# Performance work log

Hardware: AMD Instinct MI355X
Metric: run time of the kernel (lower is better)

The kernel has to match this reference:

```python
import jax, jax.numpy as jnp
import numpy as np

F = 32          # conf['num_features']
G = 96          # voxel grid extent
N_VOX = 80000   # occupied input voxels
BN_EPS = 1e-5


def _encode(c):
    c = c.astype(np.int64) + 8
    return (c[:, 0] * 512 + c[:, 1]) * 512 + c[:, 2]


def _offsets(ks, dil):
    r = np.arange(-(ks // 2), ks // 2 + 1) * dil
    return np.stack(np.meshgrid(r, r, r, indexing='ij'), -1).reshape(-1, 3)


def _build_map(in_coords, out_coords, offsets):
    # For each kernel offset k and output voxel j, find input voxel index at
    # out_coords[j] + offsets[k]; sentinel = n_in / n_out when absent.
    n_in, n_out = len(in_coords), len(out_coords)
    keys = _encode(in_coords)
    order = np.argsort(keys).astype(np.int32)
    skeys = keys[order]
    K = len(offsets)
    in_map = np.full((K, n_out), n_in, np.int32)
    out_map = np.full((K, n_out), n_out, np.int32)
    base = np.arange(n_out, dtype=np.int32)
    for k, off in enumerate(offsets):
        q = _encode(out_coords + off)
        pos = np.clip(np.searchsorted(skeys, q), 0, n_in - 1)
        valid = skeys[pos] == q
        in_map[k] = np.where(valid, order[pos], n_in)
        out_map[k] = np.where(valid, base, n_out)
    return jnp.asarray(in_map), jnp.asarray(out_map)


def setup_inputs() -> dict:
    rng = np.random.default_rng(0)
    idx = rng.choice(G ** 3, size=N_VOX, replace=False)
    coords = np.stack(np.unravel_index(idx, (G, G, G)), 1).astype(np.int64)
    c2 = np.unique(coords // 2 * 2, axis=0)   # stride-2 coords (enc1 output)
    c4 = np.unique(coords // 4 * 4, axis=0)   # stride-4 coords (c_out.C)

    m1_in, m1_out = _build_map(coords, c2, _offsets(5, 1))  # k5 s2 conv
    m2_in, m2_out = _build_map(c2, c2, _offsets(3, 2))      # enc1 blocks
    m3_in, m3_out = _build_map(c2, c4, _offsets(3, 2))      # conv2 -> c_out.C
    m4_in, m4_out = _build_map(c4, c4, _offsets(3, 4))      # enc2 blocks

    key = jax.random.key(0)
    ks = jax.random.split(key, 8)
    s = 0.05
    return {
        'x_geo': jax.random.normal(ks[0], (N_VOX, 1), jnp.float32),
        'x_col': jax.random.uniform(ks[1], (N_VOX, 3), jnp.float32),
        'w0': jax.random.normal(ks[2], (125, 4, F), jnp.float32) * s,
        'w_e1': jax.random.normal(ks[3], (2, 2, 27, F, F), jnp.float32) * s,
        'g_e1': jnp.ones((2, 2, F), jnp.float32),
        'b_e1': jnp.zeros((2, 2, F), jnp.float32),
        'w2': jax.random.normal(ks[4], (27, F, 2 * F), jnp.float32) * s,
        'w_e2': jax.random.normal(ks[5], (2, 2, 27, 2 * F, 2 * F), jnp.float32) * s,
        'g_e2': jnp.ones((2, 2, 2 * F), jnp.float32),
        'b_e2': jnp.zeros((2, 2, 2 * F), jnp.float32),
        'm1_in': m1_in, 'm1_out': m1_out,
        'm2_in': m2_in, 'm2_out': m2_out,
        'm3_in': m3_in, 'm3_out': m3_out,
        'm4_in': m4_in, 'm4_out': m4_out,
    }


def sparse_conv(feats, W, in_map, out_map):
    # gather -> GEMM -> scatter per kernel offset (lax.scan over K offsets)
    n_out = out_map.shape[1]
    fpad = jnp.concatenate([feats, jnp.zeros((1, feats.shape[1]), feats.dtype)], 0)
    out0 = jnp.zeros((n_out + 1, W.shape[2]), feats.dtype)
    def step(acc, kmw):
        im, om, w = kmw
        return acc.at[om].add(fpad[im] @ w), None
    out, _ = jax.lax.scan(step, out0, (in_map, out_map, W))
    return out[:n_out]


def batch_norm(x, g, b):
    mu = x.mean(0)
    var = ((x - mu) ** 2).mean(0)
    return (x - mu) * jax.lax.rsqrt(var + BN_EPS) * g + b


def basic_block(x, w, g, b, in_map, out_map):
    # ME BasicBlock: conv-BN-ReLU-conv-BN + residual, ReLU
    y = jax.nn.relu(batch_norm(sparse_conv(x, w[0], in_map, out_map), g[0], b[0]))
    y = batch_norm(sparse_conv(y, w[1], in_map, out_map), g[1], b[1])
    return jax.nn.relu(y + x)


def reference(x_geo, x_col, w0, w_e1, g_e1, b_e1, w2, w_e2, g_e2, b_e2,
              m1_in, m1_out, m2_in, m2_out, m3_in, m3_out, m4_in, m4_out):
    x = jnp.concatenate([x_geo, x_col], axis=1)          # ME.cat -> 4 channels
    x = jax.nn.relu(sparse_conv(x, w0, m1_in, m1_out))   # k5 s2 conv + ReLU
    for i in range(2):                                   # enc1 residual blocks
        x = basic_block(x, w_e1[i], g_e1[i], b_e1[i], m2_in, m2_out)
    x = sparse_conv(x, w2, m3_in, m3_out)                # conv2 onto c_out.C
    for i in range(2):                                   # enc2 residual blocks
        x = basic_block(x, w_e2[i], g_e2[i], b_e2[i], m4_in, m4_out)
    return x
```

## Files before the change

kernel.cpp:

```cpp
#include <hip/hip_runtime.h>
#include <hip/hip_bf16.h>


typedef float f4 __attribute__((ext_vector_type(4)));
typedef short short8 __attribute__((ext_vector_type(8)));
typedef short short4v __attribute__((ext_vector_type(4)));

#define BN_EPS 1e-5f

static inline int ceil_div(int a, int b) { return (a + b - 1) / b; }

static __device__ inline float btof(short s) {
    unsigned u = ((unsigned)(unsigned short)s) << 16;
    float f;
    __builtin_memcpy(&f, &u, 4);
    return f;
}
static __device__ inline short ftob(float f) {
    __hip_bfloat16 h = __float2bfloat16(f);
    short s;
    __builtin_memcpy(&s, &h, 2);
    return s;
}

struct Seg {
    const float* W;
    long long begin, end;
    int K, CIN, COUT;
};
struct ProArgs {
    Seg s[10];
    const float* geo;
    const float* col;
    __hip_bfloat16* x0;
    int n_vox;
    float* stats;
    __hip_bfloat16* pads[5];
    int padn[5];
    long long wf_total;
    __hip_bfloat16* Wf;
};

__global__ __launch_bounds__(256) void prologue(ProArgs pa, long long total) {
    long long e = (long long)blockIdx.x * 256 + threadIdx.x;
    if (e >= total) return;
    if (e < pa.wf_total) {
        int si = 0;
#pragma unroll
        for (int i = 0; i < 10; ++i)
            if (e >= pa.s[i].end) si = i + 1;
        const Seg sg = pa.s[si];
        long long r = e - sg.begin;
        int j = (int)(r & 7);
        int lane = (int)((r >> 3) & 63);
        long long rest = r >> 9;
        int NT = sg.COUT >> 4;
        int ntile = (int)(rest % NT);
        int chunk = (int)(rest / NT);
        int kd = chunk * 32 + ((lane >> 4) << 3) + j;
        int koff = kd / sg.CIN;
        int ci = kd % sg.CIN;
        int n = ntile * 16 + (lane & 15);
        float v = (koff < sg.K) ? sg.W[((size_t)koff * sg.CIN + ci) * sg.COUT + n] : 0.f;
        pa.Wf[e] = __float2bfloat16(v);
        return;
    }
    long long r = e - pa.wf_total;
    if (r < pa.n_vox) {
        int row = (int)r;
        pa.x0[row * 4 + 0] = __float2bfloat16(pa.geo[row]);
        pa.x0[row * 4 + 1] = __float2bfloat16(pa.col[row * 3 + 0]);
        pa.x0[row * 4 + 2] = __float2bfloat16(pa.col[row * 3 + 1]);
        pa.x0[row * 4 + 3] = __float2bfloat16(pa.col[row * 3 + 2]);
        return;
    }
    r -= pa.n_vox;
    if (r < 4096) {
        pa.stats[r] = 0.f;
        return;
    }
    r -= 4096;
#pragma unroll
    for (int i = 0; i < 5; ++i) {
        if (r < pa.padn[i]) {
            pa.pads[i][r] = __float2bfloat16(0.f);
            return;
        }
        r -= pa.padn[i];
    }
}

template <int C>
__device__ inline void bn_coef(const float* st, const float* g, const float* b,
                               int c, int n, float& sc, float& sh) {
    float rn = 1.f / (float)n;
    float sum = st[c] + st[2 * C + c] + st[4 * C + c] + st[6 * C + c];
    float sq  = st[C + c] + st[3 * C + c] + st[5 * C + c] + st[7 * C + c];
    float mu = sum * rn;
    float inv = rsqrtf(sq * rn - mu * mu + BN_EPS);
    sc = inv * g[c];
    sh = b[c] - mu * sc;
}

template <int CIN, int COUT, int MT, int K, bool BNF>
__global__ __launch_bounds__(256) void conv_splitk(
    const __hip_bfloat16* __restrict__ feat,
    const __hip_bfloat16* __restrict__ Wf,
    const int* __restrict__ in_map,
    __hip_bfloat16* __restrict__ out,
    float* __restrict__ stats,
    const float* __restrict__ in_stats,
    const float* __restrict__ in_g,
    const float* __restrict__ in_b,
    int n_out, int n_in) {
    constexpr int NT = COUT / 16;
    constexpr int H = CIN / 32;
    constexpr int R = MT * 16;
    constexpr int KPW = (K + 3) / 4;
    const int t = threadIdx.x, w = t >> 6, lane = t & 63;
    const int quad = lane >> 4, ml = lane & 15;
    const int mb = blockIdx.x * R;

    __shared__ float red[4][R][COUT];
    __shared__ float sred[2][256];
    __shared__ float isc[CIN], ish[CIN];

    if (BNF) {
        if (t < CIN) {
            float sc, sh;
            bn_coef<CIN>(in_stats, in_g, in_b, t, n_in, sc, sh);
            isc[t] = sc;
            ish[t] = sh;
        }
        __syncthreads();
    }
    float scr[H][8], shr[H][8];
    if (BNF) {
#pragma unroll
        for (int h = 0; h < H; ++h)
#pragma unroll
            for (int j = 0; j < 8; ++j) {
                int ch = h * 32 + quad * 8 + j;
                scr[h][j] = isc[ch];
                shr[h][j] = ish[ch];
            }
    }

    f4 acc[MT * NT];
#pragma unroll
    for (int i = 0; i < MT * NT; ++i) acc[i] = (f4){0.f, 0.f, 0.f, 0.f};

#pragma unroll
    for (int kk = 0; kk < KPW; ++kk) {
        const int k = kk * 4 + w;
        const int krow = (k < K) ? k : 0;
        const int* mk = in_map + (size_t)krow * n_out;
        int idx[MT];
#pragma unroll
        for (int mi = 0; mi < MT; ++mi) {
            int m = mb + mi * 16 + ml;
            idx[mi] = (m < n_out) ? mk[m] : n_in;
        }
        short8 bfrag[H * NT];
#pragma unroll
        for (int h = 0; h < H; ++h)
#pragma unroll
            for (int nt = 0; nt < NT; ++nt)
                bfrag[h * NT + nt] = *(const short8*)(
                    Wf + (((size_t)(k * H + h) * NT + nt) * 64 + lane) * 8);
#pragma unroll
        for (int mi = 0; mi < MT; ++mi) {
            const __hip_bfloat16* fp = feat + (size_t)idx[mi] * CIN + quad * 8;
            const bool sent = (idx[mi] == n_in);
#pragma unroll
            for (int h = 0; h < H; ++h) {
                short8 a = *(const short8*)(fp + h * 32);
                if (BNF) {
#pragma unroll
                    for (int j = 0; j < 8; ++j) {
                        float f = btof(a[j]) * scr[h][j] + shr[h][j];
                        f = fmaxf(f, 0.f);
                        a[j] = sent ? (short)0 : ftob(f);
                    }
                }
#pragma unroll
                for (int nt = 0; nt < NT; ++nt)
                    acc[mi * NT + nt] = __builtin_amdgcn_mfma_f32_16x16x32_bf16(
                        a, bfrag[h * NT + nt], acc[mi * NT + nt], 0, 0, 0);
            }
        }
    }

#pragma unroll
    for (int mi = 0; mi < MT; ++mi)
#pragma unroll
        for (int nt = 0; nt < NT; ++nt)
#pragma unroll
            for (int i = 0; i < 4; ++i)
                red[w][mi * 16 + quad * 4 + i][nt * 16 + ml] = acc[mi * NT + nt][i];
    __syncthreads();

    constexpr int E = (R * COUT) / 256;
    constexpr int RSTEP = 256 / COUT;
    const int col = t % COUT;
    const int rg = t / COUT;
    float s = 0.f, s2 = 0.f;
#pragma unroll
    for (int i = 0; i < E; ++i) {
        int r = rg + i * RSTEP;
        float v = red[0][r][col] + red[1][r][col] + red[2][r][col] + red[3][r][col];
        s += v;
        s2 += v * v;
        int grow = mb + r;
        if (grow < n_out) out[(size_t)grow * COUT + col] = __float2bfloat16(v);
    }

    if (stats) {
        sred[0][t] = s;
        sred[1][t] = s2;
        __syncthreads();
        if (t < 2 * COUT) {
            int c = t % COUT;
            int which = t / COUT;
            float v = 0.f;
#pragma unroll
            for (int j = 0; j < RSTEP; ++j) v += sred[which][j * COUT + c];
            atomicAdd(&stats[((blockIdx.x & 3) * 2 + which) * COUT + c], v);
        }
    }
}

__global__ __launch_bounds__(256) void stem_mfma(
    const __hip_bfloat16* __restrict__ feat,
    const __hip_bfloat16* __restrict__ Wf,
    const int* __restrict__ in_map,
    __hip_bfloat16* __restrict__ out,
    int n_out, int n_in) {
    const int t = threadIdx.x, w = t >> 6, lane = t & 63;
    const int quad = lane >> 4, ml = lane & 15;
    const int ntile = w & 1, mgroup = w >> 1;
    const int mb = blockIdx.x * 64 + mgroup * 32;
    const int m0 = mb + ml, m1 = mb + 16 + ml;
    const bool v0 = m0 < n_out, v1 = m1 < n_out;

    f4 acc0 = {0.f, 0.f, 0.f, 0.f};
    f4 acc1 = {0.f, 0.f, 0.f, 0.f};

#pragma unroll 4
    for (int chunk = 0; chunk < 16; ++chunk) {
        int k0 = chunk * 8 + quad * 2;
        int k1 = k0 + 1;
        int k0c = (k0 < 125) ? k0 : 0;
        int k1c = (k1 < 125) ? k1 : 0;
        short8 b = *(const short8*)(Wf + ((size_t)(chunk * 2 + ntile) * 64 + lane) * 8);
        int ia = v0 ? in_map[(size_t)k0c * n_out + m0] : n_in;
        int ib = v0 ? in_map[(size_t)k1c * n_out + m0] : n_in;
        int ic = v1 ? in_map[(size_t)k0c * n_out + m1] : n_in;
        int id = v1 ? in_map[(size_t)k1c * n_out + m1] : n_in;
        short4v pa = *(const short4v*)(feat + (size_t)ia * 4);
        short4v pb = *(const short4v*)(feat + (size_t)ib * 4);
        short4v pc = *(const short4v*)(feat + (size_t)ic * 4);
        short4v pd = *(const short4v*)(feat + (size_t)id * 4);
        short8 a0, a1;
        a0[0] = pa[0]; a0[1] = pa[1]; a0[2] = pa[2]; a0[3] = pa[3];
        a0[4] = pb[0]; a0[5] = pb[1]; a0[6] = pb[2]; a0[7] = pb[3];
        a1[0] = pc[0]; a1[1] = pc[1]; a1[2] = pc[2]; a1[3] = pc[3];
        a1[4] = pd[0]; a1[5] = pd[1]; a1[6] = pd[2]; a1[7] = pd[3];
        acc0 = __builtin_amdgcn_mfma_f32_16x16x32_bf16(a0, b, acc0, 0, 0, 0);
        acc1 = __builtin_amdgcn_mfma_f32_16x16x32_bf16(a1, b, acc1, 0, 0, 0);
    }

    const int col = ntile * 16 + ml;
#pragma unroll
    for (int i = 0; i < 4; ++i) {
        int r0 = mb + quad * 4 + i;
        if (r0 < n_out)
            out[(size_t)r0 * 32 + col] = __float2bfloat16(fmaxf(acc0[i], 0.f));
        int r1 = mb + 16 + quad * 4 + i;
        if (r1 < n_out)
            out[(size_t)r1 * 32 + col] = __float2bfloat16(fmaxf(acc1[i], 0.f));
    }
}

template <int C>
__global__ __launch_bounds__(256) void bn_res8_bf16(
    const __hip_bfloat16* __restrict__ y, const __hip_bfloat16* __restrict__ res,
    const float* __restrict__ st, const float* __restrict__ g,
    const float* __restrict__ b, __hip_bfloat16* __restrict__ out, int n) {
    __shared__ float sc[C], sh[C];
    const int t = threadIdx.x;
    if (t < C) bn_coef<C>(st, g, b, t, n, sc[t], sh[t]);
    __syncthreads();
    long long i = (long long)blockIdx.x * 256 + t;
    long long tot = (long long)n * (C / 8);
    if (i >= tot) return;
    int c0 = (int)(i % (C / 8)) * 8;
    short8 v = *(const short8*)(y + i * 8);
    short8 r = *(const short8*)(res + i * 8);
    short8 o;
#pragma unroll
    for (int j = 0; j < 8; ++j) {
        float f = btof(v[j]) * sc[c0 + j] + sh[c0 + j] + btof(r[j]);
        o[j] = ftob(fmaxf(f, 0.f));
    }
    *(short8*)(out + i * 8) = o;
}

template <int C>
__global__ __launch_bounds__(256) void bn_res8_f32(
    const __hip_bfloat16* __restrict__ y, const __hip_bfloat16* __restrict__ res,
    const float* __restrict__ st, const float* __restrict__ g,
    const float* __restrict__ b, float* __restrict__ out, int n) {
    __shared__ float sc[C], sh[C];
    const int t = threadIdx.x;
    if (t < C) bn_coef<C>(st, g, b, t, n, sc[t], sh[t]);
    __syncthreads();
    long long i = (long long)blockIdx.x * 256 + t;
    long long tot = (long long)n * (C / 8);
    if (i >= tot) return;
    int c0 = (int)(i % (C / 8)) * 8;
    short8 v = *(const short8*)(y + i * 8);
    short8 r = *(const short8*)(res + i * 8);
    f4 o0, o1;
#pragma unroll
    for (int j = 0; j < 8; ++j) {
        float f = btof(v[j]) * sc[c0 + j] + sh[c0 + j] + btof(r[j]);
        f = fmaxf(f, 0.f);
        if (j < 4) o0[j] = f; else o1[j - 4] = f;
    }
    *(f4*)(out + i * 8) = o0;
    *(f4*)(out + i * 8 + 4) = o1;
}

extern "C" void kernel_launch(void* const* d_in, const int* in_sizes, int n_in_cnt,
                              void* d_out, int out_size, void* d_ws, size_t ws_size,
                              hipStream_t stream) {
    const float* x_geo = (const float*)d_in[0];
    const float* x_col = (const float*)d_in[1];
    const float* w0    = (const float*)d_in[2];
    const float* w_e1  = (const float*)d_in[3];
    const float* g_e1  = (const float*)d_in[4];
    const float* b_e1  = (const float*)d_in[5];
    const float* w2    = (const float*)d_in[6];
    const float* w_e2  = (const float*)d_in[7];
    const float* g_e2  = (const float*)d_in[8];
    const float* b_e2  = (const float*)d_in[9];
    const int* m1_in = (const int*)d_in[10];
    const int* m2_in = (const int*)d_in[12];
    const int* m3_in = (const int*)d_in[14];
    const int* m4_in = (const int*)d_in[16];

    const int n_vox = in_sizes[0];
    const int nc2 = in_sizes[10] / 125;
    const int nc4 = in_sizes[14] / 27;
    (void)out_size; (void)ws_size; (void)n_in_cnt;

    char* p = (char*)d_ws;
    auto alloc = [&](size_t bytes) -> char* {
        char* r = p;
        p += (bytes + 255) & ~(size_t)255;
        return r;
    };
    float* stats = (float*)alloc(8 * 512 * sizeof(float));
    __hip_bfloat16* x0 = (__hip_bfloat16*)alloc((size_t)(n_vox + 1) * 4 * 2);
    __hip_bfloat16* A  = (__hip_bfloat16*)alloc((size_t)(nc2 + 1) * 32 * 2);
    __hip_bfloat16* B  = (__hip_bfloat16*)alloc((size_t)(nc2 + 1) * 32 * 2);
    __hip_bfloat16* Cb = (__hip_bfloat16*)alloc((size_t)(nc2 + 1) * 32 * 2);
    __hip_bfloat16* D  = (__hip_bfloat16*)alloc((size_t)(nc4 + 1) * 64 * 2);
    __hip_bfloat16* E  = (__hip_bfloat16*)alloc((size_t)(nc4 + 1) * 64 * 2);
    __hip_bfloat16* Fb = (__hip_bfloat16*)alloc((size_t)(nc4 + 1) * 64 * 2);

    const long long sz_stem = 16LL * 2 * 512;
    const long long sz_e1   = 28LL * 2 * 512;
    const long long sz_c2   = 28LL * 4 * 512;
    const long long sz_e2   = 56LL * 4 * 512;
    const long long wf_total = sz_stem + 4 * sz_e1 + sz_c2 + 4 * sz_e2;
    __hip_bfloat16* Wf = (__hip_bfloat16*)alloc((size_t)wf_total * 2);

    long long off_stem = 0;
    long long off_e1[4], off_e2[4];
    long long cur = sz_stem;
    for (int i = 0; i < 4; ++i) { off_e1[i] = cur; cur += sz_e1; }
    long long off_c2 = cur; cur += sz_c2;
    for (int i = 0; i < 4; ++i) { off_e2[i] = cur; cur += sz_e2; }

    ProArgs pa;
    cur = 0;
    auto seg = [&](int i, const float* W, int K, int CIN, int COUT, long long n) {
        pa.s[i].W = W; pa.s[i].K = K; pa.s[i].CIN = CIN; pa.s[i].COUT = COUT;
        pa.s[i].begin = cur; pa.s[i].end = cur + n; cur += n;
    };
    seg(0, w0, 125, 4, 32, sz_stem);
    for (int i = 0; i < 4; ++i)
        seg(1 + i, w_e1 + (size_t)i * 27 * 32 * 32, 27, 32, 32, sz_e1);
    seg(5, w2, 27, 32, 64, sz_c2);
    for (int i = 0; i < 4; ++i)
        seg(6 + i, w_e2 + (size_t)i * 27 * 64 * 64, 27, 64, 64, sz_e2);
    pa.geo = x_geo; pa.col = x_col; pa.x0 = x0; pa.n_vox = n_vox;
    pa.stats = stats;
    pa.pads[0] = x0 + (size_t)n_vox * 4; pa.padn[0] = 4;
    pa.pads[1] = A + (size_t)nc2 * 32;   pa.padn[1] = 32;
    pa.pads[2] = B + (size_t)nc2 * 32;   pa.padn[2] = 32;
    pa.pads[3] = D + (size_t)nc4 * 64;   pa.padn[3] = 64;
    pa.pads[4] = E + (size_t)nc4 * 64;   pa.padn[4] = 64;
    pa.wf_total = wf_total;
    pa.Wf = Wf;
    long long pro_total = wf_total + n_vox + 4096 + (4 + 32 + 32 + 64 + 64);
    prologue<<<ceil_div((int)pro_total, 256), 256, 0, stream>>>(pa, pro_total);

    stem_mfma<<<ceil_div(nc2, 64), 256, 0, stream>>>(x0, Wf + off_stem, m1_in, A,
                                                     nc2, n_vox);

    int slot = 0;
    for (int blk = 0; blk < 2; ++blk) {
        const float* gA = g_e1 + (blk * 2 + 0) * 32, *bA = b_e1 + (blk * 2 + 0) * 32;
        const float* gB = g_e1 + (blk * 2 + 1) * 32, *bB = b_e1 + (blk * 2 + 1) * 32;
        conv_splitk<32, 32, 2, 27, false><<<ceil_div(nc2, 32), 256, 0, stream>>>(
            A, Wf + off_e1[blk * 2 + 0], m2_in, B, stats + slot * 512,
            nullptr, nullptr, nullptr, nc2, nc2);
        conv_splitk<32, 32, 2, 27, true><<<ceil_div(nc2, 32), 256, 0, stream>>>(
            B, Wf + off_e1[blk * 2 + 1], m2_in, Cb, stats + (slot + 1) * 512,
            stats + slot * 512, gA, bA, nc2, nc2);
        bn_res8_bf16<32><<<ceil_div(nc2 * 4, 256), 256, 0, stream>>>(
            Cb, A, stats + (slot + 1) * 512, gB, bB, A, nc2);
        slot += 2;
    }

    conv_splitk<32, 64, 1, 27, false><<<ceil_div(nc4, 16), 256, 0, stream>>>(
        A, Wf + off_c2, m3_in, D, nullptr,
        nullptr, nullptr, nullptr, nc4, nc2);

    for (int blk = 0; blk < 2; ++blk) {
        const float* gA = g_e2 + (blk * 2 + 0) * 64, *bA = b_e2 + (blk * 2 + 0) * 64;
        const float* gB = g_e2 + (blk * 2 + 1) * 64, *bB = b_e2 + (blk * 2 + 1) * 64;
        conv_splitk<64, 64, 1, 27, false><<<ceil_div(nc4, 16), 256, 0, stream>>>(
            D, Wf + off_e2[blk * 2 + 0], m4_in, E, stats + slot * 512,
            nullptr, nullptr, nullptr, nc4, nc4);
        conv_splitk<64, 64, 1, 27, true><<<ceil_div(nc4, 16), 256, 0, stream>>>(
            E, Wf + off_e2[blk * 2 + 1], m4_in, Fb, stats + (slot + 1) * 512,
            stats + slot * 512, gA, bA, nc4, nc4);
        if (blk == 0) {
            bn_res8_bf16<64><<<ceil_div(nc4 * 8, 256), 256, 0, stream>>>(
                Fb, D, stats + (slot + 1) * 512, gB, bB, D, nc4);
        } else {
            bn_res8_f32<64><<<ceil_div(nc4 * 8, 256), 256, 0, stream>>>(
                Fb, D, stats + (slot + 1) * 512, gB, bB, (float*)d_out, nc4);
        }
        slot += 2;
    }
}
```

Measured before the change: 341.6 us.

## Fuse all pipeline stages into one cooperative persistent megakernel with grid sync

```diff
diff --git a/kernel.cpp b/kernel.cpp
--- a/kernel.cpp
+++ b/kernel.cpp
@@ -1,5 +1,8 @@
 #include <hip/hip_runtime.h>
 #include <hip/hip_bf16.h>
+#include <hip/hip_cooperative_groups.h>
+
+namespace cg = cooperative_groups;
 
 
 typedef float f4 __attribute__((ext_vector_type(4)));
@@ -9,6 +12,7 @@
 #define BN_EPS 1e-5f
 
 static inline int ceil_div(int a, int b) { return (a + b - 1) / b; }
+__device__ static inline int dceil(int a, int b) { return (a + b - 1) / b; }
 
 static __device__ inline float btof(short s) {
     unsigned u = ((unsigned)(unsigned short)s) << 16;
@@ -28,7 +32,8 @@
     long long begin, end;
     int K, CIN, COUT;
 };
-struct ProArgs {
+
+struct MegaArgs {
     Seg s[10];
     const float* geo;
     const float* col;
@@ -38,57 +43,16 @@
     __hip_bfloat16* pads[5];
     int padn[5];
     long long wf_total;
+    long long pro_total;
     __hip_bfloat16* Wf;
+    __hip_bfloat16 *A, *B, *Cb, *D, *E, *Fb;
+    float* outf;
+    const int *m1, *m2, *m3, *m4;
+    const float *g_e1, *b_e1, *g_e2, *b_e2;
+    long long off_stem, off_c2;
+    long long off_e1[4], off_e2[4];
+    int nc2, nc4;
 };
-
-__global__ __launch_bounds__(256) void prologue(ProArgs pa, long long total) {
-    long long e = (long long)blockIdx.x * 256 + threadIdx.x;
-    if (e >= total) return;
-    if (e < pa.wf_total) {
-        int si = 0;
-#pragma unroll
-        for (int i = 0; i < 10; ++i)
-            if (e >= pa.s[i].end) si = i + 1;
-        const Seg sg = pa.s[si];
-        long long r = e - sg.begin;
-        int j = (int)(r & 7);
-        int lane = (int)((r >> 3) & 63);
-        long long rest = r >> 9;
-        int NT = sg.COUT >> 4;
-        int ntile = (int)(rest % NT);
-        int chunk = (int)(rest / NT);
-        int kd = chunk * 32 + ((lane >> 4) << 3) + j;
-        int koff = kd / sg.CIN;
-        int ci = kd % sg.CIN;
-        int n = ntile * 16 + (lane & 15);
-        float v = (koff < sg.K) ? sg.W[((size_t)koff * sg.CIN + ci) * sg.COUT + n] : 0.f;
-        pa.Wf[e] = __float2bfloat16(v);
-        return;
-    }
-    long long r = e - pa.wf_total;
-    if (r < pa.n_vox) {
-        int row = (int)r;
-        pa.x0[row * 4 + 0] = __float2bfloat16(pa.geo[row]);
-        pa.x0[row * 4 + 1] = __float2bfloat16(pa.col[row * 3 + 0]);
-        pa.x0[row * 4 + 2] = __float2bfloat16(pa.col[row * 3 + 1]);
-        pa.x0[row * 4 + 3] = __float2bfloat16(pa.col[row * 3 + 2]);
-        return;
-    }
-    r -= pa.n_vox;
-    if (r < 4096) {
-        pa.stats[r] = 0.f;
-        return;
-    }
-    r -= 4096;
-#pragma unroll
-    for (int i = 0; i < 5; ++i) {
-        if (r < pa.padn[i]) {
-            pa.pads[i][r] = __float2bfloat16(0.f);
-            return;
-        }
-        r -= pa.padn[i];
-    }
-}
 
 template <int C>
 __device__ inline void bn_coef(const float* st, const float* g, const float* b,
@@ -102,234 +66,364 @@
     sh = b[c] - mu * sc;
 }
 
+__device__ void do_prologue(const MegaArgs& pa) {
+    for (long long e = (long long)blockIdx.x * 256 + threadIdx.x; e < pa.pro_total;
+         e += (long long)gridDim.x * 256) {
+        if (e < pa.wf_total) {
+            int si = 0;
+#pragma unroll
+            for (int i = 0; i < 10; ++i)
+                if (e >= pa.s[i].end) si = i + 1;
+            const Seg sg = pa.s[si];
+            long long r = e - sg.begin;
+            int j = (int)(r & 7);
+            int lane = (int)((r >> 3) & 63);
+            long long rest = r >> 9;
+            int NT = sg.COUT >> 4;
+            int ntile = (int)(rest % NT);
+            int chunk = (int)(rest / NT);
+            int kd = chunk * 32 + ((lane >> 4) << 3) + j;
+            int koff = kd / sg.CIN;
+            int ci = kd % sg.CIN;
+            int n = ntile * 16 + (lane & 15);
+            float v = (koff < sg.K) ? sg.W[((size_t)koff * sg.CIN + ci) * sg.COUT + n] : 0.f;
+            pa.Wf[e] = __float2bfloat16(v);
+            continue;
+        }
+        long long r = e - pa.wf_total;
+        if (r < pa.n_vox) {
+            int row = (int)r;
+            pa.x0[row * 4 + 0] = __float2bfloat16(pa.geo[row]);
+            pa.x0[row * 4 + 1] = __float2bfloat16(pa.col[row * 3 + 0]);
+            pa.x0[row * 4 + 2] = __float2bfloat16(pa.col[row * 3 + 1]);
+            pa.x0[row * 4 + 3] = __float2bfloat16(pa.col[row * 3 + 2]);
+            continue;
+        }
+        r -= pa.n_vox;
+        if (r < 4096) {
+            pa.stats[r] = 0.f;
+            continue;
+        }
+        r -= 4096;
+#pragma unroll
+        for (int i = 0; i < 5; ++i) {
+            if (r < pa.padn[i]) {
+                pa.pads[i][r] = __float2bfloat16(0.f);
+                r = -1;
+                break;
+            }
+            r -= pa.padn[i];
+        }
+    }
+}
+
+__device__ void stage_stem(const MegaArgs& a) {
+    const int t = threadIdx.x, w = t >> 6, lane = t & 63;
+    const int quad = lane >> 4, ml = lane & 15;
+    const int ntile = w & 1, mgroup = w >> 1;
+    const int n_out = a.nc2, n_in = a.n_vox;
+    const __hip_bfloat16* feat = a.x0;
+    const __hip_bfloat16* Wf = a.Wf + a.off_stem;
+    const int* in_map = a.m1;
+    __hip_bfloat16* out = a.A;
+    const int ntiles = dceil(n_out, 64);
+    for (int tile = blockIdx.x; tile < ntiles; tile += gridDim.x) {
+        const int mb = tile * 64 + mgroup * 32;
+        const int m0 = mb + ml, m1 = mb + 16 + ml;
+        const bool v0 = m0 < n_out, v1 = m1 < n_out;
+        f4 acc0 = {0.f, 0.f, 0.f, 0.f};
+        f4 acc1 = {0.f, 0.f, 0.f, 0.f};
+#pragma unroll 2
+        for (int chunk = 0; chunk < 16; ++chunk) {
+            int k0 = chunk * 8 + quad * 2;
+            int k1 = k0 + 1;
+            int k0c = (k0 < 125) ? k0 : 0;
+            int k1c = (k1 < 125) ? k1 : 0;
+            short8 b = *(const short8*)(Wf + ((size_t)(chunk * 2 + ntile) * 64 + lane) * 8);
+            int ia = v0 ? in_map[(size_t)k0c * n_out + m0] : n_in;
+            int ib = v0 ? in_map[(size_t)k1c * n_out + m0] : n_in;
+            int ic = v1 ? in_map[(size_t)k0c * n_out + m1] : n_in;
+            int id = v1 ? in_map[(size_t)k1c * n_out + m1] : n_in;
+            short4v p0 = *(const short4v*)(feat + (size_t)ia * 4);
+            short4v p1 = *(const short4v*)(feat + (size_t)ib * 4);
+            short4v p2 = *(const short4v*)(feat + (size_t)ic * 4);
+            short4v p3 = *(const short4v*)(feat + (size_t)id * 4);
+            short8 a0, a1;
+            a0[0] = p0[0]; a0[1] = p0[1]; a0[2] = p0[2]; a0[3] = p0[3];
+            a0[4] = p1[0]; a0[5] = p1[1]; a0[6] = p1[2]; a0[7] = p1[3];
+            a1[0] = p2[0]; a1[1] = p2[1]; a1[2] = p2[2]; a1[3] = p2[3];
+            a1[4] = p3[0]; a1[5] = p3[1]; a1[6] = p3[2]; a1[7] = p3[3];
+            acc0 = __builtin_amdgcn_mfma_f32_16x16x32_bf16(a0, b, acc0, 0, 0, 0);
+            acc1 = __builtin_amdgcn_mfma_f32_16x16x32_bf16(a1, b, acc1, 0, 0, 0);
+        }
+        const int col = ntile * 16 + ml;
+#pragma unroll
+        for (int i = 0; i < 4; ++i) {
+            int r0 = mb + quad * 4 + i;
+            if (r0 < n_out)
+                out[(size_t)r0 * 32 + col] = __float2bfloat16(fmaxf(acc0[i], 0.f));
+            int r1 = mb + 16 + quad * 4 + i;
+            if (r1 < n_out)
+                out[(size_t)r1 * 32 + col] = __float2bfloat16(fmaxf(acc1[i], 0.f));
+        }
+    }
+}
+
 template <int CIN, int COUT, int MT, int K, bool BNF>
-__global__ __launch_bounds__(256) void conv_splitk(
-    const __hip_bfloat16* __restrict__ feat,
-    const __hip_bfloat16* __restrict__ Wf,
-    const int* __restrict__ in_map,
-    __hip_bfloat16* __restrict__ out,
-    float* __restrict__ stats,
-    const float* __restrict__ in_stats,
-    const float* __restrict__ in_g,
-    const float* __restrict__ in_b,
-    int n_out, int n_in) {
+__device__ void stage_conv(const __hip_bfloat16* __restrict__ feat,
+                           const __hip_bfloat16* __restrict__ Wf,
+                           const int* __restrict__ in_map,
+                           __hip_bfloat16* __restrict__ out,
+                           float* __restrict__ stats,
+                           const float* __restrict__ in_stats,
+                           const float* __restrict__ in_g,
+                           const float* __restrict__ in_b,
+                           int n_out, int n_in,
+                           float* red, float* sred, float* ibn) {
     constexpr int NT = COUT / 16;
     constexpr int H = CIN / 32;
     constexpr int R = MT * 16;
     constexpr int KPW = (K + 3) / 4;
     const int t = threadIdx.x, w = t >> 6, lane = t & 63;
     const int quad = lane >> 4, ml = lane & 15;
-    const int mb = blockIdx.x * R;
-
-    __shared__ float red[4][R][COUT];
-    __shared__ float sred[2][256];
-    __shared__ float isc[CIN], ish[CIN];
-
-    if (BNF) {
+
+    if constexpr (BNF) {
         if (t < CIN) {
             float sc, sh;
             bn_coef<CIN>(in_stats, in_g, in_b, t, n_in, sc, sh);
-            isc[t] = sc;
-            ish[t] = sh;
+            ibn[t] = sc;
+            ibn[CIN + t] = sh;
         }
         __syncthreads();
     }
     float scr[H][8], shr[H][8];
-    if (BNF) {
+    if constexpr (BNF) {
 #pragma unroll
         for (int h = 0; h < H; ++h)
 #pragma unroll
             for (int j = 0; j < 8; ++j) {
                 int ch = h * 32 + quad * 8 + j;
-                scr[h][j] = isc[ch];
-                shr[h][j] = ish[ch];
-            }
-    }
-
-    f4 acc[MT * NT];
-#pragma unroll
-    for (int i = 0; i < MT * NT; ++i) acc[i] = (f4){0.f, 0.f, 0.f, 0.f};
-
-#pragma unroll
-    for (int kk = 0; kk < KPW; ++kk) {
-        const int k = kk * 4 + w;
-        const int krow = (k < K) ? k : 0;
-        const int* mk = in_map + (size_t)krow * n_out;
-        int idx[MT];
-#pragma unroll
-        for (int mi = 0; mi < MT; ++mi) {
-            int m = mb + mi * 16 + ml;
-            idx[mi] = (m < n_out) ? mk[m] : n_in;
-        }
-        short8 bfrag[H * NT];
-#pragma unroll
-        for (int h = 0; h < H; ++h)
+                scr[h][j] = ibn[ch];
+                shr[h][j] = ibn[CIN + ch];
+            }
+    }
+
+    const int ntiles = dceil(n_out, R);
+    for (int tile = blockIdx.x; tile < ntiles; tile += gridDim.x) {
+        const int mb = tile * R;
+        f4 acc[MT * NT];
+#pragma unroll
+        for (int i = 0; i < MT * NT; ++i) acc[i] = (f4){0.f, 0.f, 0.f, 0.f};
+
+#pragma unroll
+        for (int kk = 0; kk < KPW; ++kk) {
+            const int k = kk * 4 + w;
+            const int krow = (k < K) ? k : 0;
+            const int* mk = in_map + (size_t)krow * n_out;
+            int idx[MT];
+#pragma unroll
+            for (int mi = 0; mi < MT; ++mi) {
+                int m = mb + mi * 16 + ml;
+                idx[mi] = (m < n_out) ? mk[m] : n_in;
+            }
+            short8 bfrag[H * NT];
+#pragma unroll
+            for (int h = 0; h < H; ++h)
+#pragma unroll
+                for (int nt = 0; nt < NT; ++nt)
+                    bfrag[h * NT + nt] = *(const short8*)(
+                        Wf + (((size_t)(k * H + h) * NT + nt) * 64 + lane) * 8);
+#pragma unroll
+            for (int mi = 0; mi < MT; ++mi) {
+                const __hip_bfloat16* fp = feat + (size_t)idx[mi] * CIN + quad * 8;
+                const bool sent = (idx[mi] == n_in);
+#pragma unroll
+                for (int h = 0; h < H; ++h) {
+                    short8 av = *(const short8*)(fp + h * 32);
+                    if constexpr (BNF) {
+#pragma unroll
+                        for (int j = 0; j < 8; ++j) {
+                            float f = btof(av[j]) * scr[h][j] + shr[h][j];
+                            f = fmaxf(f, 0.f);
+                            av[j] = sent ? (short)0 : ftob(f);
+                        }
+                    }
+#pragma unroll
+                    for (int nt = 0; nt < NT; ++nt)
+                        acc[mi * NT + nt] = __builtin_amdgcn_mfma_f32_16x16x32_bf16(
+                            av, bfrag[h * NT + nt], acc[mi * NT + nt], 0, 0, 0);
+                }
+            }
+        }
+
+#pragma unroll
+        for (int mi = 0; mi < MT; ++mi)
 #pragma unroll
             for (int nt = 0; nt < NT; ++nt)
-                bfrag[h * NT + nt] = *(const short8*)(
-                    Wf + (((size_t)(k * H + h) * NT + nt) * 64 + lane) * 8);
-#pragma unroll
-        for (int mi = 0; mi < MT; ++mi) {
-            const __hip_bfloat16* fp = feat + (size_t)idx[mi] * CIN + quad * 8;
-            const bool sent = (idx[mi] == n_in);
-#pragma unroll
-            for (int h = 0; h < H; ++h) {
-                short8 a = *(const short8*)(fp + h * 32);
-                if (BNF) {
-#pragma unroll
-                    for (int j = 0; j < 8; ++j) {
-                        float f = btof(a[j]) * scr[h][j] + shr[h][j];
-                        f = fmaxf(f, 0.f);
-                        a[j] = sent ? (short)0 : ftob(f);
-                    }
-                }
-#pragma unroll
-                for (int nt = 0; nt < NT; ++nt)
-                    acc[mi * NT + nt] = __builtin_amdgcn_mfma_f32_16x16x32_bf16(
-                        a, bfrag[h * NT + nt], acc[mi * NT + nt], 0, 0, 0);
-            }
-        }
-    }
-
-#pragma unroll
-    for (int mi = 0; mi < MT; ++mi)
-#pragma unroll
-        for (int nt = 0; nt < NT; ++nt)
-#pragma unroll
-            for (int i = 0; i < 4; ++i)
-                red[w][mi * 16 + quad * 4 + i][nt * 16 + ml] = acc[mi * NT + nt][i];
+#pragma unroll
+                for (int i = 0; i < 4; ++i)
+                    red[((size_t)w * R + mi * 16 + quad * 4 + i) * COUT + nt * 16 + ml] =
+                        acc[mi * NT + nt][i];
+        __syncthreads();
+
+        constexpr int E = (R * COUT) / 256;
+        constexpr int RSTEP = 256 / COUT;
+        const int col = t % COUT;
+        const int rg = t / COUT;
+        float s = 0.f, s2 = 0.f;
+#pragma unroll
+        for (int i = 0; i < E; ++i) {
+            int r = rg + i * RSTEP;
+            float v = red[(0 * R + r) * COUT + col] + red[(1 * R + r) * COUT + col] +
+                      red[(2 * R + r) * COUT + col] + red[(3 * R + r) * COUT + col];
+            s += v;
+            s2 += v * v;
+            int grow = mb + r;
+            if (grow < n_out) out[(size_t)grow * COUT + col] = __float2bfloat16(v);
+        }
+
+        if (stats) {
+            sred[t] = s;
+            sred[256 + t] = s2;
+            __syncthreads();
+            if (t < 2 * COUT) {
+                int c = t % COUT;
+                int which = t / COUT;
+                float v = 0.f;
+#pragma unroll
+                for (int j = 0; j < RSTEP; ++j) v += sred[which * 256 + j * COUT + c];
+                atomicAdd(&stats[((tile & 3) * 2 + which) * COUT + c], v);
+            }
+        }
+        __syncthreads();
+    }
+}
+
+template <int C, bool F32OUT>
+__device__ void stage_bnres(const __hip_bfloat16* __restrict__ y,
+                            const __hip_bfloat16* __restrict__ res,
+                            const float* __restrict__ st,
+                            const float* __restrict__ g,
+                            const float* __restrict__ b,
+                            void* outp, int n, float* ibn) {
+    const int t = threadIdx.x;
+    if (t < C) {
+        float sc, sh;
+        bn_coef<C>(st, g, b, t, n, sc, sh);
+        ibn[t] = sc;
+        ibn[C + t] = sh;
+    }
     __syncthreads();
-
-    constexpr int E = (R * COUT) / 256;
-    constexpr int RSTEP = 256 / COUT;
-    const int col = t % COUT;
-    const int rg = t / COUT;
-    float s = 0.f, s2 = 0.f;
-#pragma unroll
-    for (int i = 0; i < E; ++i) {
-        int r = rg + i * RSTEP;
-        float v = red[0][r][col] + red[1][r][col] + red[2][r][col] + red[3][r][col];
-        s += v;
-        s2 += v * v;
-        int grow = mb + r;
-        if (grow < n_out) out[(size_t)grow * COUT + col] = __float2bfloat16(v);
-    }
-
-    if (stats) {
-        sred[0][t] = s;
-        sred[1][t] = s2;
-        __syncthreads();
-        if (t < 2 * COUT) {
-            int c = t % COUT;
-            int which = t / COUT;
-            float v = 0.f;
-#pragma unroll
-            for (int j = 0; j < RSTEP; ++j) v += sred[which][j * COUT + c];
-            atomicAdd(&stats[((blockIdx.x & 3) * 2 + which) * COUT + c], v);
-        }
-    }
-}
-
-__global__ __launch_bounds__(256) void stem_mfma(
-    const __hip_bfloat16* __restrict__ feat,
-    const __hip_bfloat16* __restrict__ Wf,
-    const int* __restrict__ in_map,
-    __hip_bfloat16* __restrict__ out,
-    int n_out, int n_in) {
-    const int t = threadIdx.x, w = t >> 6, lane = t & 63;
-    const int quad = lane >> 4, ml = lane & 15;
-    const int ntile = w & 1, mgroup = w >> 1;
-    const int mb = blockIdx.x * 64 + mgroup * 32;
-    const int m0 = mb + ml, m1 = mb + 16 + ml;
-    const bool v0 = m0 < n_out, v1 = m1 < n_out;
-
-    f4 acc0 = {0.f, 0.f, 0.f, 0.f};
-    f4 acc1 = {0.f, 0.f, 0.f, 0.f};
-
-#pragma unroll 4
-    for (int chunk = 0; chunk < 16; ++chunk) {
-        int k0 = chunk * 8 + quad * 2;
-        int k1 = k0 + 1;
-        int k0c = (k0 < 125) ? k0 : 0;
-        int k1c = (k1 < 125) ? k1 : 0;
-        short8 b = *(const short8*)(Wf + ((size_t)(chunk * 2 + ntile) * 64 + lane) * 8);
-        int ia = v0 ? in_map[(size_t)k0c * n_out + m0] : n_in;
-        int ib = v0 ? in_map[(size_t)k1c * n_out + m0] : n_in;
-        int ic = v1 ? in_map[(size_t)k0c * n_out + m1] : n_in;
-        int id = v1 ? in_map[(size_t)k1c * n_out + m1] : n_in;
-        short4v pa = *(const short4v*)(feat + (size_t)ia * 4);
-        short4v pb = *(const short4v*)(feat + (size_t)ib * 4);
-        short4v pc = *(const short4v*)(feat + (size_t)ic * 4);
-        short4v pd = *(const short4v*)(feat + (size_t)id * 4);
-        short8 a0, a1;
-        a0[0] = pa[0]; a0[1] = pa[1]; a0[2] = pa[2]; a0[3] = pa[3];
-        a0[4] = pb[0]; a0[5] = pb[1]; a0[6] = pb[2]; a0[7] = pb[3];
-        a1[0] = pc[0]; a1[1] = pc[1]; a1[2] = pc[2]; a1[3] = pc[3];
-        a1[4] = pd[0]; a1[5] = pd[1]; a1[6] = pd[2]; a1[7] = pd[3];
-        acc0 = __builtin_amdgcn_mfma_f32_16x16x32_bf16(a0, b, acc0, 0, 0, 0);
-        acc1 = __builtin_amdgcn_mfma_f32_16x16x32_bf16(a1, b, acc1, 0, 0, 0);
-    }
-
-    const int col = ntile * 16 + ml;
-#pragma unroll
-    for (int i = 0; i < 4; ++i) {
-        int r0 = mb + quad * 4 + i;
-        if (r0 < n_out)
-            out[(size_t)r0 * 32 + col] = __float2bfloat16(fmaxf(acc0[i], 0.f));
-        int r1 = mb + 16 + quad * 4 + i;
-        if (r1 < n_out)
-            out[(size_t)r1 * 32 + col] = __float2bfloat16(fmaxf(acc1[i], 0.f));
-    }
-}
-
-template <int C>
-__global__ __launch_bounds__(256) void bn_res8_bf16(
-    const __hip_bfloat16* __restrict__ y, const __hip_bfloat16* __restrict__ res,
-    const float* __restrict__ st, const float* __restrict__ g,
-    const float* __restrict__ b, __hip_bfloat16* __restrict__ out, int n) {
-    __shared__ float sc[C], sh[C];
-    const int t = threadIdx.x;
-    if (t < C) bn_coef<C>(st, g, b, t, n, sc[t], sh[t]);
-    __syncthreads();
-    long long i = (long long)blockIdx.x * 256 + t;
     long long tot = (long long)n * (C / 8);
-    if (i >= tot) return;
-    int c0 = (int)(i % (C / 8)) * 8;
-    short8 v = *(const short8*)(y + i * 8);
-    short8 r = *(const short8*)(res + i * 8);
-    short8 o;
-#pragma unroll
-    for (int j = 0; j < 8; ++j) {
-        float f = btof(v[j]) * sc[c0 + j] + sh[c0 + j] + btof(r[j]);
-        o[j] = ftob(fmaxf(f, 0.f));
-    }
-    *(short8*)(out + i * 8) = o;
-}
-
-template <int C>
-__global__ __launch_bounds__(256) void bn_res8_f32(
-    const __hip_bfloat16* __restrict__ y, const __hip_bfloat16* __restrict__ res,
-    const float* __restrict__ st, const float* __restrict__ g,
-    const float* __restrict__ b, float* __restrict__ out, int n) {
-    __shared__ float sc[C], sh[C];
-    const int t = threadIdx.x;
-    if (t < C) bn_coef<C>(st, g, b, t, n, sc[t], sh[t]);
-    __syncthreads();
-    long long i = (long long)blockIdx.x * 256 + t;
-    long long tot = (long long)n * (C / 8);
-    if (i >= tot) return;
-    int c0 = (int)(i % (C / 8)) * 8;
-    short8 v = *(const short8*)(y + i * 8);
-    short8 r = *(const short8*)(res + i * 8);
-    f4 o0, o1;
-#pragma unroll
-    for (int j = 0; j < 8; ++j) {
-        float f = btof(v[j]) * sc[c0 + j] + sh[c0 + j] + btof(r[j]);
-        f = fmaxf(f, 0.f);
-        if (j < 4) o0[j] = f; else o1[j - 4] = f;
-    }
-    *(f4*)(out + i * 8) = o0;
-    *(f4*)(out + i * 8 + 4) = o1;
+    for (long long i = (long long)blockIdx.x * 256 + t; i < tot;
+         i += (long long)gridDim.x * 256) {
+        int c0 = (int)(i % (C / 8)) * 8;
+        short8 v = *(const short8*)(y + i * 8);
+        short8 r = *(const short8*)(res + i * 8);
+        if constexpr (F32OUT) {
+            float* out = (float*)outp;
+            f4 o0, o1;
+#pragma unroll
+            for (int j = 0; j < 8; ++j) {
+                float f = btof(v[j]) * ibn[c0 + j] + ibn[C + c0 + j] + btof(r[j]);
+                f = fmaxf(f, 0.f);
+                if (j < 4) o0[j] = f; else o1[j - 4] = f;
+            }
+            *(f4*)(out + i * 8) = o0;
+            *(f4*)(out + i * 8 + 4) = o1;
+        } else {
+            __hip_bfloat16* out = (__hip_bfloat16*)outp;
+            short8 o;
+#pragma unroll
+            for (int j = 0; j < 8; ++j) {
+                float f = btof(v[j]) * ibn[c0 + j] + ibn[C + c0 + j] + btof(r[j]);
+                o[j] = ftob(fmaxf(f, 0.f));
+            }
+            *(short8*)(out + i * 8) = o;
+        }
+    }
+}
+
+__global__ __launch_bounds__(256) void mega(MegaArgs a) {
+    cg::grid_group grid = cg::this_grid();
+    __shared__ float red[4096];
+    __shared__ float sred[512];
+    __shared__ float ibn[128];
+
+    do_prologue(a);
+    grid.sync();
+    stage_stem(a);
+    grid.sync();
+
+    stage_conv<32, 32, 2, 27, false>(a.A, a.Wf + a.off_e1[0], a.m2, a.B,
+        a.stats + 0 * 512, nullptr, nullptr, nullptr, a.nc2, a.nc2, red, sred, ibn);
+    grid.sync();
+    stage_conv<32, 32, 2, 27, true>(a.B, a.Wf + a.off_e1[1], a.m2, a.Cb,
+        a.stats + 1 * 512, a.stats + 0 * 512, a.g_e1 + 0, a.b_e1 + 0,
+        a.nc2, a.nc2, red, sred, ibn);
+    grid.sync();
+    stage_bnres<32, false>(a.Cb, a.A, a.stats + 1 * 512, a.g_e1 + 32, a.b_e1 + 32,
+                           a.A, a.nc2, ibn);
+    grid.sync();
+
+    stage_conv<32, 32, 2, 27, false>(a.A, a.Wf + a.off_e1[2], a.m2, a.B,
+        a.stats + 2 * 512, nullptr, nullptr, nullptr, a.nc2, a.nc2, red, sred, ibn);
+    grid.sync();
+    stage_conv<32, 32, 2, 27, true>(a.B, a.Wf + a.off_e1[3], a.m2, a.Cb,
+        a.stats + 3 * 512, a.stats + 2 * 512, a.g_e1 + 64, a.b_e1 + 64,
+        a.nc2, a.nc2, red, sred, ibn);
+    grid.sync();
+    stage_bnres<32, false>(a.Cb, a.A, a.stats + 3 * 512, a.g_e1 + 96, a.b_e1 + 96,
+                           a.A, a.nc2, ibn);
+    grid.sync();
+
+    stage_conv<32, 64, 1, 27, false>(a.A, a.Wf + a.off_c2, a.m3, a.D,
+        nullptr, nullptr, nullptr, nullptr, a.nc4, a.nc2, red, sred, ibn);
+    grid.sync();
+
+    stage_conv<64, 64, 1, 27, false>(a.D, a.Wf + a.off_e2[0], a.m4, a.E,
+        a.stats + 4 * 512, nullptr, nullptr, nullptr, a.nc4, a.nc4, red, sred, ibn);
+    grid.sync();
+    stage_conv<64, 64, 1, 27, true>(a.E, a.Wf + a.off_e2[1], a.m4, a.Fb,
+        a.stats + 5 * 512, a.stats + 4 * 512, a.g_e2 + 0, a.b_e2 + 0,
+        a.nc4, a.nc4, red, sred, ibn);
+    grid.sync();
+    stage_bnres<64, false>(a.Fb, a.D, a.stats + 5 * 512, a.g_e2 + 64, a.b_e2 + 64,
+                           a.D, a.nc4, ibn);
+    grid.sync();
+
+    stage_conv<64, 64, 1, 27, false>(a.D, a.Wf + a.off_e2[2], a.m4, a.E,
+        a.stats + 6 * 512, nullptr, nullptr, nullptr, a.nc4, a.nc4, red, sred, ibn);
+    grid.sync();
+    stage_conv<64, 64, 1, 27, true>(a.E, a.Wf + a.off_e2[3], a.m4, a.Fb,
+        a.stats + 7 * 512, a.stats + 6 * 512, a.g_e2 + 128, a.b_e2 + 128,
+        a.nc4, a.nc4, red, sred, ibn);
+    grid.sync();
+    stage_bnres<64, true>(a.Fb, a.D, a.stats + 7 * 512, a.g_e2 + 192, a.b_e2 + 192,
+                          a.outf, a.nc4, ibn);
+}
+
+__global__ __launch_bounds__(256) void k_prologue(MegaArgs a) { do_prologue(a); }
+__global__ __launch_bounds__(256) void k_stem(MegaArgs a) { stage_stem(a); }
+
+template <int CIN, int COUT, int MT, int K, bool BNF>
+__global__ __launch_bounds__(256) void k_conv(
+    const __hip_bfloat16* feat, const __hip_bfloat16* Wf, const int* in_map,
+    __hip_bfloat16* out, float* stats, const float* ist, const float* ig,
+    const float* ib, int n_out, int n_in) {
+    __shared__ float red[4096];
+    __shared__ float sred[512];
+    __shared__ float ibn[128];
+    stage_conv<CIN, COUT, MT, K, BNF>(feat, Wf, in_map, out, stats, ist, ig, ib,
+                                      n_out, n_in, red, sred, ibn);
+}
+
+template <int C, bool F32OUT>
+__global__ __launch_bounds__(256) void k_bnres(
+    const __hip_bfloat16* y, const __hip_bfloat16* res, const float* st,
+    const float* g, const float* b, void* out, int n) {
+    __shared__ float ibn[128];
+    stage_bnres<C, F32OUT>(y, res, st, g, b, out, n, ibn);
 }
 
 extern "C" void kernel_launch(void* const* d_in, const int* in_sizes, int n_in_cnt,
@@ -345,10 +439,6 @@
     const float* w_e2  = (const float*)d_in[7];
     const float* g_e2  = (const float*)d_in[8];
     const float* b_e2  = (const float*)d_in[9];
-    const int* m1_in = (const int*)d_in[10];
-    const int* m2_in = (const int*)d_in[12];
-    const int* m3_in = (const int*)d_in[14];
-    const int* m4_in = (const int*)d_in[16];
 
     const int n_vox = in_sizes[0];
     const int nc2 = in_sizes[10] / 125;
@@ -377,18 +467,11 @@
     const long long wf_total = sz_stem + 4 * sz_e1 + sz_c2 + 4 * sz_e2;
     __hip_bfloat16* Wf = (__hip_bfloat16*)alloc((size_t)wf_total * 2);
 
-    long long off_stem = 0;
-    long long off_e1[4], off_e2[4];
-    long long cur = sz_stem;
-    for (int i = 0; i < 4; ++i) { off_e1[i] = cur; cur += sz_e1; }
-    long long off_c2 = cur; cur += sz_c2;
-    for (int i = 0; i < 4; ++i) { off_e2[i] = cur; cur += sz_e2; }
-
-    ProArgs pa;
-    cur = 0;
+    MegaArgs ma;
+    long long cur = 0;
     auto seg = [&](int i, const float* W, int K, int CIN, int COUT, long long n) {
-        pa.s[i].W = W; pa.s[i].K = K; pa.s[i].CIN = CIN; pa.s[i].COUT = COUT;
-        pa.s[i].begin = cur; pa.s[i].end = cur + n; cur += n;
+        ma.s[i].W = W; ma.s[i].K = K; ma.s[i].CIN = CIN; ma.s[i].COUT = COUT;
+        ma.s[i].begin = cur; ma.s[i].end = cur + n; cur += n;
     };
     seg(0, w0, 125, 4, 32, sz_stem);
     for (int i = 0; i < 4; ++i)
@@ -396,56 +479,90 @@
     seg(5, w2, 27, 32, 64, sz_c2);
     for (int i = 0; i < 4; ++i)
         seg(6 + i, w_e2 + (size_t)i * 27 * 64 * 64, 27, 64, 64, sz_e2);
-    pa.geo = x_geo; pa.col = x_col; pa.x0 = x0; pa.n_vox = n_vox;
-    pa.stats = stats;
-    pa.pads[0] = x0 + (size_t)n_vox * 4; pa.padn[0] = 4;
-    pa.pads[1] = A + (size_t)nc2 * 32;   pa.padn[1] = 32;
-    pa.pads[2] = B + (size_t)nc2 * 32;   pa.padn[2] = 32;
-    pa.pads[3] = D + (size_t)nc4 * 64;   pa.padn[3] = 64;
-    pa.pads[4] = E + (size_t)nc4 * 64;   pa.padn[4] = 64;
-    pa.wf_total = wf_total;
-    pa.Wf = Wf;
-    long long pro_total = wf_total + n_vox + 4096 + (4 + 32 + 32 + 64 + 64);
-    prologue<<<ceil_div((int)pro_total, 256), 256, 0, stream>>>(pa, pro_total);
-
-    stem_mfma<<<ceil_div(nc2, 64), 256, 0, stream>>>(x0, Wf + off_stem, m1_in, A,
-                                                     nc2, n_vox);
-
-    int slot = 0;
-    for (int blk = 0; blk < 2; ++blk) {
-        const float* gA = g_e1 + (blk * 2 + 0) * 32, *bA = b_e1 + (blk * 2 + 0) * 32;
-        const float* gB = g_e1 + (blk * 2 + 1) * 32, *bB = b_e1 + (blk * 2 + 1) * 32;
-        conv_splitk<32, 32, 2, 27, false><<<ceil_div(nc2, 32), 256, 0, stream>>>(
-            A, Wf + off_e1[blk * 2 + 0], m2_in, B, stats + slot * 512,
-            nullptr, nullptr, nullptr, nc2, nc2);
-        conv_splitk<32, 32, 2, 27, true><<<ceil_div(nc2, 32), 256, 0, stream>>>(
-            B, Wf + off_e1[blk * 2 + 1], m2_in, Cb, stats + (slot + 1) * 512,
-            stats + slot * 512, gA, bA, nc2, nc2);
-        bn_res8_bf16<32><<<ceil_div(nc2 * 4, 256), 256, 0, stream>>>(
-            Cb, A, stats + (slot + 1) * 512, gB, bB, A, nc2);
-        slot += 2;
-    }
-
-    conv_splitk<32, 64, 1, 27, false><<<ceil_div(nc4, 16), 256, 0, stream>>>(
-        A, Wf + off_c2, m3_in, D, nullptr,
+
+    ma.off_stem = 0;
+    cur = sz_stem;
+    for (int i = 0; i < 4; ++i) { ma.off_e1[i] = cur; cur += sz_e1; }
+    ma.off_c2 = cur; cur += sz_c2;
+    for (int i = 0; i < 4; ++i) { ma.off_e2[i] = cur; cur += sz_e2; }
+
+    ma.geo = x_geo; ma.col = x_col; ma.x0 = x0; ma.n_vox = n_vox;
+    ma.stats = stats;
+    ma.pads[0] = x0 + (size_t)n_vox * 4; ma.padn[0] = 4;
+    ma.pads[1] = A + (size_t)nc2 * 32;   ma.padn[1] = 32;
+    ma.pads[2] = B + (size_t)nc2 * 32;   ma.padn[2] = 32;
+    ma.pads[3] = D + (size_t)nc4 * 64;   ma.padn[3] = 64;
+    ma.pads[4] = E + (size_t)nc4 * 64;   ma.padn[4] = 64;
+    ma.wf_total = wf_total;
+    ma.pro_total = wf_total + n_vox + 4096 + (4 + 32 + 32 + 64 + 64);
+    ma.Wf = Wf;
+    ma.A = A; ma.B = B; ma.Cb = Cb; ma.D = D; ma.E = E; ma.Fb = Fb;
+    ma.outf = (float*)d_out;
+    ma.m1 = (const int*)d_in[10];
+    ma.m2 = (const int*)d_in[12];
+    ma.m3 = (const int*)d_in[14];
+    ma.m4 = (const int*)d_in[16];
+    ma.g_e1 = g_e1; ma.b_e1 = b_e1; ma.g_e2 = g_e2; ma.b_e2 = b_e2;
+    ma.nc2 = nc2; ma.nc4 = nc4;
+
+    bool coop_done = false;
+    int maxPerCU = 0;
+    hipError_t qe = hipOccupancyMaxActiveBlocksPerMultiprocessor(
+        &maxPerCU, (const void*)mega, 256, 0);
+    int nCU = 0;
+    int dev = 0;
+    hipGetDevice(&dev);
+    hipDeviceGetAttribute(&nCU, hipDeviceAttributeMultiprocessorCount, dev);
+    if (qe == hipSuccess && maxPerCU > 0 && nCU > 0) {
+        int grid = maxPerCU * nCU;
+        void* kargs[] = { &ma };
+        hipError_t le = hipLaunchCooperativeKernel((void*)mega, dim3(grid),
+                                                   dim3(256), kargs, 0, stream);
+        if (le == hipSuccess) coop_done = true;
+        else (void)hipGetLastError();
+    }
+    if (coop_done) return;
+
+    k_prologue<<<ceil_div((int)ma.pro_total, 256), 256, 0, stream>>>(ma);
+    k_stem<<<ceil_div(nc2, 64), 256, 0, stream>>>(ma);
+
+    k_conv<32, 32, 2, 27, false><<<ceil_div(nc2, 32), 256, 0, stream>>>(
+        A, Wf + ma.off_e1[0], ma.m2, B, stats + 0 * 512,
+        nullptr, nullptr, nullptr, nc2, nc2);
+    k_conv<32, 32, 2, 27, true><<<ceil_div(nc2, 32), 256, 0, stream>>>(
+        B, Wf + ma.off_e1[1], ma.m2, Cb, stats + 1 * 512,
+        stats + 0 * 512, g_e1 + 0, b_e1 + 0, nc2, nc2);
+    k_bnres<32, false><<<ceil_div(nc2 * 4, 256), 256, 0, stream>>>(
+        Cb, A, stats + 1 * 512, g_e1 + 32, b_e1 + 32, A, nc2);
+
+    k_conv<32, 32, 2, 27, false><<<ceil_div(nc2, 32), 256, 0, stream>>>(
+        A, Wf + ma.off_e1[2], ma.m2, B, stats + 2 * 512,
+        nullptr, nullptr, nullptr, nc2, nc2);
+    k_conv<32, 32, 2, 27, true><<<ceil_div(nc2, 32), 256, 0, stream>>>(
+        B, Wf + ma.off_e1[3], ma.m2, Cb, stats + 3 * 512,
+        stats + 2 * 512, g_e1 + 64, b_e1 + 64, nc2, nc2);
+    k_bnres<32, false><<<ceil_div(nc2 * 4, 256), 256, 0, stream>>>(
+        Cb, A, stats + 3 * 512, g_e1 + 96, b_e1 + 96, A, nc2);
+
+    k_conv<32, 64, 1, 27, false><<<ceil_div(nc4, 16), 256, 0, stream>>>(
+        A, Wf + ma.off_c2, ma.m3, D, nullptr,
         nullptr, nullptr, nullptr, nc4, nc2);
 
-    for (int blk = 0; blk < 2; ++blk) {
-        const float* gA = g_e2 + (blk * 2 + 0) * 64, *bA = b_e2 + (blk * 2 + 0) * 64;
-        const float* gB = g_e2 + (blk * 2 + 1) * 64, *bB = b_e2 + (blk * 2 + 1) * 64;
-        conv_splitk<64, 64, 1, 27, false><<<ceil_div(nc4, 16), 256, 0, stream>>>(
-            D, Wf + off_e2[blk * 2 + 0], m4_in, E, stats + slot * 512,
-            nullptr, nullptr, nullptr, nc4, nc4);
-        conv_splitk<64, 64, 1, 27, true><<<ceil_div(nc4, 16), 256, 0, stream>>>(
-            E, Wf + off_e2[blk * 2 + 1], m4_in, Fb, stats + (slot + 1) * 512,
-            stats + slot * 512, gA, bA, nc4, nc4);
-        if (blk == 0) {
-            bn_res8_bf16<64><<<ceil_div(nc4 * 8, 256), 256, 0, stream>>>(
-                Fb, D, stats + (slot + 1) * 512, gB, bB, D, nc4);
-        } else {
-            bn_res8_f32<64><<<ceil_div(nc4 * 8, 256), 256, 0, stream>>>(
-                Fb, D, stats + (slot + 1) * 512, gB, bB, (float*)d_out, nc4);
-        }
-        slot += 2;
-    }
-}
+    k_conv<64, 64, 1, 27, false><<<ceil_div(nc4, 16), 256, 0, stream>>>(
+        D, Wf + ma.off_e2[0], ma.m4, E, stats + 4 * 512,
+        nullptr, nullptr, nullptr, nc4, nc4);
+    k_conv<64, 64, 1, 27, true><<<ceil_div(nc4, 16), 256, 0, stream>>>(
+        E, Wf + ma.off_e2[1], ma.m4, Fb, stats + 5 * 512,
+        stats + 4 * 512, g_e2 + 0, b_e2 + 0, nc4, nc4);
+    k_bnres<64, false><<<ceil_div(nc4 * 8, 256), 256, 0, stream>>>(
+        Fb, D, stats + 5 * 512, g_e2 + 64, b_e2 + 64, D, nc4);
+
+    k_conv<64, 64, 1, 27, false><<<ceil_div(nc4, 16), 256, 0, stream>>>(
+        D, Wf + ma.off_e2[2], ma.m4, E, stats + 6 * 512,
+        nullptr, nullptr, nullptr, nc4, nc4);
+    k_conv<64, 64, 1, 27, true><<<ceil_div(nc4, 16), 256, 0, stream>>>(
+        E, Wf + ma.off_e2[3], ma.m4, Fb, stats + 7 * 512,
+        stats + 6 * 512, g_e2 + 128, b_e2 + 128, nc4, nc4);
+    k_bnres<64, true><<<ceil_div(nc4 * 8, 256), 256, 0, stream>>>(
+        Fb, D, stats + 7 * 512, g_e2 + 192, b_e2 + 192, (float*)d_out, nc4);
+}
```

Result: slower. 622.3 us (+82.1%).
